# Kernel optimization log

Measured on AMD Instinct MI355X. Metric: run time of the kernel, lower is better.

Reference implementation:

```python
import jax, jax.numpy as jnp
import numpy as np

EMBED = 1024
HEADS = 16
HEAD_DIM = EMBED // HEADS
RANK = 8
ALPHA = 16
SCALE_LORA = ALPHA / RANK  # 2.0


def _lora_linear(x, W, b, A, B):
    # F.linear(x, W, b) + scale * F.linear(F.linear(x, A), B)
    return x @ W.T + b + SCALE_LORA * ((x @ A.T) @ B.T)


def setup_inputs() -> dict:
    key = jax.random.key(0)
    ks = jax.random.split(key, 17)
    d = {"x": jax.random.normal(ks[0], (2, 2048, EMBED), dtype=jnp.float32)}
    names = ["q", "k", "v", "o"]
    i = 1
    for n in names:
        d[f"W{n}"] = jax.random.normal(ks[i], (EMBED, EMBED), dtype=jnp.float32) * 0.02; i += 1
        d[f"b{n}"] = jnp.zeros((EMBED,), dtype=jnp.float32)
        d[f"A{n}"] = jax.random.normal(ks[i], (RANK, EMBED), dtype=jnp.float32) * 0.02; i += 1
        d[f"B{n}"] = jax.random.normal(ks[i], (EMBED, RANK), dtype=jnp.float32) * 0.02; i += 1
    return d


def reference(x, Wq, bq, Aq, Bq, Wk, bk, Ak, Bk, Wv, bv, Av, Bv, Wo, bo, Ao, Bo):
    N, S, _ = x.shape
    Q = _lora_linear(x, Wq, bq, Aq, Bq).reshape(N, S, HEADS, HEAD_DIM)
    K = _lora_linear(x, Wk, bk, Ak, Bk).reshape(N, S, HEADS, HEAD_DIM)
    V = _lora_linear(x, Wv, bv, Av, Bv).reshape(N, S, HEADS, HEAD_DIM)
    # energy: [N, H, Sq, Sk]
    energy = jnp.einsum("nqhd,nkhd->nhqk", Q, K) / jnp.sqrt(jnp.float32(HEAD_DIM))
    attn = jax.nn.softmax(energy, axis=-1)
    out = jnp.einsum("nhqk,nkhd->nqhd", attn, V).reshape(N, S, EMBED)
    return _lora_linear(out, Wo, bo, Ao, Bo)
```

## Files before the change

kernel.cpp:

```cpp
#include <hip/hip_runtime.h>
#include <stdint.h>

typedef uint16_t u16;
typedef short s16x8 __attribute__((ext_vector_type(8)));
typedef float f32x4 __attribute__((ext_vector_type(4)));
typedef unsigned short u16x4 __attribute__((ext_vector_type(4)));
typedef uint32_t u32;
typedef u32 u32x2 __attribute__((ext_vector_type(2)));
typedef u32 u32x4 __attribute__((ext_vector_type(4)));

#define MFMA16(a,b,c) __builtin_amdgcn_mfma_f32_16x16x32_bf16((a),(b),(c),0,0,0)
#define QSCALE 0.18033688011112042f

__device__ __forceinline__ float b2f(u16 b){
  union { u32 u; float f; } v; v.u = ((u32)b)<<16; return v.f;
}
__device__ __forceinline__ u16 f2b(float f){
  union { float f; u32 u; } v; v.f = f;
  return (u16)((v.u + 0x7fffu + ((v.u>>16)&1u))>>16);
}
__device__ __forceinline__ u32 fbits(float f){
  union { float f; u32 u; } v; v.f = f; return v.u;
}
__device__ __forceinline__ void load_lds_16B(const void* g, void* l){
  __builtin_amdgcn_global_load_lds((const __attribute__((address_space(1))) void*)g,
                                   (__attribute__((address_space(3))) void*)l, 16, 0, 0);
}

template<bool XF32, int NMAT>
__global__ __launch_bounds__(256) void lora_conv_kernel(
    const void* __restrict__ Xv,
    const float* __restrict__ A0, const float* __restrict__ A1, const float* __restrict__ A2,
    float* __restrict__ T0, float* __restrict__ T1, float* __restrict__ T2,
    u16* __restrict__ xb,
    const float* __restrict__ W0, const float* __restrict__ W1,
    const float* __restrict__ W2, const float* __restrict__ W3,
    u16* __restrict__ Wb)
{
  if (XF32 && blockIdx.x >= 1024){
    const int cv = blockIdx.x - 1024;
    const int y = cv>>8;
    const float* src = (y==0)?W0:(y==1)?W1:(y==2)?W2:W3;
    u16* dst = Wb + (size_t)y*1048576;
    const int g = (cv&255)*256 + threadIdx.x;
#pragma unroll
    for (int t=0;t<4;t++){
      const int i4 = g + t*65536;
      const f32x4 v = *(const f32x4*)(src + (size_t)i4*4);
      u16x4 o;
#pragma unroll
      for (int j=0;j<4;j++) o[j] = f2b(v[j]);
      *(u16x4*)(dst + (size_t)i4*4) = o;
    }
    return;
  }

  const int wid = threadIdx.x>>6, lane = threadIdx.x&63;
  const int m = blockIdx.x*4 + wid;

  float xf[16];
  if (XF32){
    const float* xp = (const float*)Xv + (size_t)m*1024 + lane*16;
#pragma unroll
    for (int q=0;q<4;q++){
      const f32x4 v = *(const f32x4*)(xp + q*4);
#pragma unroll
      for (int j=0;j<4;j++) xf[q*4+j] = v[j];
    }
    u16* xbp = xb + (size_t)m*1024 + lane*16;
#pragma unroll
    for (int q=0;q<4;q++){
      u16x4 o;
#pragma unroll
      for (int j=0;j<4;j++) o[j] = f2b(xf[q*4+j]);
      *(u16x4*)(xbp + q*4) = o;
    }
  } else {
    const u16* xp = (const u16*)Xv + (size_t)m*1024 + lane*16;
#pragma unroll
    for (int j=0;j<16;j++) xf[j] = b2f(xp[j]);
  }

#pragma unroll
  for (int mat=0; mat<NMAT; mat++){
    const float* A = (mat==0)?A0:(mat==1)?A1:A2;
    float* T = (mat==0)?T0:(mat==1)?T1:T2;
    float accv[8];
#pragma unroll
    for (int r=0;r<8;r++){
      const float* ap = A + r*1024 + lane*16;
      float s = 0.f;
#pragma unroll
      for (int q=0;q<4;q++){
        const f32x4 av = *(const f32x4*)(ap + q*4);
#pragma unroll
        for (int j=0;j<4;j++) s += xf[q*4+j]*av[j];
      }
      accv[r] = s;
    }
#pragma unroll
    for (int r=0;r<8;r++){
      float s = accv[r];
      s += __shfl_xor(s,1);  s += __shfl_xor(s,2);  s += __shfl_xor(s,4);
      s += __shfl_xor(s,8);  s += __shfl_xor(s,16); s += __shfl_xor(s,32);
      accv[r] = s;
    }
    if (lane==0){
#pragma unroll
      for (int r=0;r<8;r++) T[(size_t)m*8 + r] = accv[r];
    }
  }
}

__global__ __launch_bounds__(256,2) void gemm_qkv_kernel(
    const u16* __restrict__ Xb, const u16* __restrict__ Wb,
    const float* __restrict__ bq, const float* __restrict__ bk, const float* __restrict__ bv,
    const float* __restrict__ tq, const float* __restrict__ tk, const float* __restrict__ tv,
    const float* __restrict__ Blq, const float* __restrict__ Blk, const float* __restrict__ Blv,
    u16* __restrict__ Qb, u16* __restrict__ Kb, u16* __restrict__ Vtb)
{
  __shared__ u16 At[128*32];
  __shared__ u16 Bt[128*32];
  const int tid = threadIdx.x;
  const int wid = tid>>6, lane = tid&63;
  const int quad = lane>>4, l16 = lane&15;
  const int wm = wid>>1, wn = wid&1;
  const int proj = blockIdx.x>>3;
  const int n0 = (blockIdx.x&7)<<7, m0 = blockIdx.y<<7;
  const u16* W = Wb + (size_t)proj*1048576;
  const float* bias = (proj==0)?bq:(proj==1)?bk:bv;
  const float* T    = (proj==0)?tq:(proj==1)?tk:tv;
  const float* Bl   = (proj==0)?Blq:(proj==1)?Blk:Blv;
  const float scale = (proj==0)?QSCALE:1.0f;

  f32x4 acc[4][4];
#pragma unroll
  for (int i=0;i<4;i++)
#pragma unroll
    for (int j=0;j<4;j++) acc[i][j] = f32x4{0.f,0.f,0.f,0.f};

  for (int k0=0;k0<1024;k0+=32){
#pragma unroll
    for (int p=0;p<2;p++){
      const int s = wid*128 + p*64 + lane;
      const int row = s>>2, c = s&3;
      load_lds_16B(Xb + (size_t)(m0+row)*1024 + k0 + c*8, At + (wid*128+p*64)*8);
      load_lds_16B(W  + (size_t)(n0+row)*1024 + k0 + c*8, Bt + (wid*128+p*64)*8);
    }
    __syncthreads();
    s16x8 af[4], bfr[4];
#pragma unroll
    for (int t=0;t<4;t++){
      const int r = wm*64 + t*16 + l16;
      af[t]  = *(const s16x8*)(At + r*32 + quad*8);
      const int c = wn*64 + t*16 + l16;
      bfr[t] = *(const s16x8*)(Bt + c*32 + quad*8);
    }
#pragma unroll
    for (int tm=0;tm<4;tm++)
#pragma unroll
      for (int tn=0;tn<4;tn++)
        acc[tm][tn] = MFMA16(af[tm], bfr[tn], acc[tm][tn]);
    __syncthreads();
  }

  s16x8 tf[4], bfl[4];
#pragma unroll
  for (int t=0;t<4;t++){ tf[t] = s16x8{0,0,0,0,0,0,0,0}; bfl[t] = s16x8{0,0,0,0,0,0,0,0}; }
  if (quad==0){
#pragma unroll
    for (int tm=0;tm<4;tm++){
      const float* tp = T + (size_t)(m0 + wm*64 + tm*16 + l16)*8;
      const f32x4 a0 = *(const f32x4*)(tp);
      const f32x4 a1 = *(const f32x4*)(tp+4);
#pragma unroll
      for (int j=0;j<4;j++){ tf[tm][j] = (short)f2b(2.0f*a0[j]); tf[tm][4+j] = (short)f2b(2.0f*a1[j]); }
    }
#pragma unroll
    for (int tn=0;tn<4;tn++){
      const float* bp = Bl + (size_t)(n0 + wn*64 + tn*16 + l16)*8;
      const f32x4 b0 = *(const f32x4*)(bp);
      const f32x4 b1 = *(const f32x4*)(bp+4);
#pragma unroll
      for (int j=0;j<4;j++){ bfl[tn][j] = (short)f2b(b0[j]); bfl[tn][4+j] = (short)f2b(b1[j]); }
    }
  }
#pragma unroll
  for (int tm=0;tm<4;tm++)
#pragma unroll
    for (int tn=0;tn<4;tn++)
      acc[tm][tn] = MFMA16(tf[tm], bfl[tn], acc[tm][tn]);

#pragma unroll
  for (int tn=0;tn<4;tn++){
    const int n = n0 + wn*64 + tn*16 + l16;
    const float bn = bias[n];
#pragma unroll
    for (int tm=0;tm<4;tm++){
      const int mb = m0 + wm*64 + tm*16 + quad*4;
      if (proj==0){
#pragma unroll
        for (int rg=0;rg<4;rg++) Qb[(size_t)(mb+rg)*1024 + n] = f2b((acc[tm][tn][rg]+bn)*scale);
      } else if (proj==1){
#pragma unroll
        for (int rg=0;rg<4;rg++) Kb[(size_t)(mb+rg)*1024 + n] = f2b(acc[tm][tn][rg]+bn);
      } else {
        const int batch = mb>>11, sI = mb&2047;
        const int hh = n>>6, dd = n&63;
        u16x4 pk;
#pragma unroll
        for (int rg=0;rg<4;rg++) pk[rg] = f2b(acc[tm][tn][rg]+bn);
        *(u16x4*)(Vtb + (size_t)((batch*16+hh)*64+dd)*2048 + sI) = pk;
      }
    }
  }
}

__global__ __launch_bounds__(256,2) void gemm_o_kernel(
    const u16* __restrict__ Xb, const u16* __restrict__ W,
    const float* __restrict__ bias, const float* __restrict__ T,
    const float* __restrict__ Bl, float* __restrict__ Out)
{
  __shared__ u16 At[128*32];
  __shared__ u16 Bt[64*32];
  const int tid = threadIdx.x;
  const int wid = tid>>6, lane = tid&63;
  const int quad = lane>>4, l16 = lane&15;
  const int wm = wid>>1, wn = wid&1;
  const int m0 = blockIdx.y<<7, n0 = blockIdx.x<<6;

  f32x4 acc[4][2];
#pragma unroll
  for (int i=0;i<4;i++)
#pragma unroll
    for (int j=0;j<2;j++) acc[i][j] = f32x4{0.f,0.f,0.f,0.f};

  for (int k0=0;k0<1024;k0+=32){
#pragma unroll
    for (int p=0;p<2;p++){
      const int s = wid*128 + p*64 + lane;
      const int row = s>>2, c = s&3;
      load_lds_16B(Xb + (size_t)(m0+row)*1024 + k0 + c*8, At + (wid*128+p*64)*8);
    }
    { const int s = wid*64 + lane;
      const int row = s>>2, c = s&3;
      load_lds_16B(W + (size_t)(n0+row)*1024 + k0 + c*8, Bt + (wid*64)*8); }
    __syncthreads();
    s16x8 af[4], bfr[2];
#pragma unroll
    for (int t=0;t<4;t++){
      const int r = wm*64 + t*16 + l16;
      af[t] = *(const s16x8*)(At + r*32 + quad*8);
    }
#pragma unroll
    for (int t=0;t<2;t++){
      const int c = wn*32 + t*16 + l16;
      bfr[t] = *(const s16x8*)(Bt + c*32 + quad*8);
    }
#pragma unroll
    for (int tm=0;tm<4;tm++)
#pragma unroll
      for (int tn=0;tn<2;tn++)
        acc[tm][tn] = MFMA16(af[tm], bfr[tn], acc[tm][tn]);
    __syncthreads();
  }

  s16x8 tf[4], bfl[2];
#pragma unroll
  for (int t=0;t<4;t++) tf[t] = s16x8{0,0,0,0,0,0,0,0};
#pragma unroll
  for (int t=0;t<2;t++) bfl[t] = s16x8{0,0,0,0,0,0,0,0};
  if (quad==0){
#pragma unroll
    for (int tm=0;tm<4;tm++){
      const float* tp = T + (size_t)(m0 + wm*64 + tm*16 + l16)*8;
      const f32x4 a0 = *(const f32x4*)(tp);
      const f32x4 a1 = *(const f32x4*)(tp+4);
#pragma unroll
      for (int j=0;j<4;j++){ tf[tm][j] = (short)f2b(2.0f*a0[j]); tf[tm][4+j] = (short)f2b(2.0f*a1[j]); }
    }
#pragma unroll
    for (int tn=0;tn<2;tn++){
      const float* bp = Bl + (size_t)(n0 + wn*32 + tn*16 + l16)*8;
      const f32x4 b0 = *(const f32x4*)(bp);
      const f32x4 b1 = *(const f32x4*)(bp+4);
#pragma unroll
      for (int j=0;j<4;j++){ bfl[tn][j] = (short)f2b(b0[j]); bfl[tn][4+j] = (short)f2b(b1[j]); }
    }
  }
#pragma unroll
  for (int tm=0;tm<4;tm++)
#pragma unroll
    for (int tn=0;tn<2;tn++)
      acc[tm][tn] = MFMA16(tf[tm], bfl[tn], acc[tm][tn]);

#pragma unroll
  for (int tn=0;tn<2;tn++){
    const int n = n0 + wn*32 + tn*16 + l16;
    const float bn = bias[n];
#pragma unroll
    for (int tm=0;tm<4;tm++){
      const int mb = m0 + wm*64 + tm*16 + quad*4;
#pragma unroll
      for (int rg=0;rg<4;rg++)
        Out[(size_t)(mb+rg)*1024 + n] = acc[tm][tn][rg] + bn;
    }
  }
}

__global__ __launch_bounds__(512,4) void attn_kernel(
    const u16* __restrict__ Q, const u16* __restrict__ K,
    const u16* __restrict__ Vt, u16* __restrict__ Out)
{
  __shared__ u16 KtB[2][128*72];
  __shared__ u16 VtB[2][64*136];
  const int tid = threadIdx.x;
  const int wid = tid>>6, lane = tid&63;
  const int quad = lane>>4, l16 = lane&15;
  const int q0 = blockIdx.x<<7;
  const int h = blockIdx.y, nb = blockIdx.z;
  const int qg = wid>>1;
  const int kh = wid&1;
  const int qw = qg*32;

  s16x8 qf[2][2];
#pragma unroll
  for (int g=0;g<2;g++){
    const int row = q0 + qw + g*16 + l16;
#pragma unroll
    for (int dh=0;dh<2;dh++)
      qf[g][dh] = *(const s16x8*)(Q + (size_t)(nb*2048+row)*1024 + h*64 + dh*32 + quad*8);
  }
  f32x4 OT[2][4];
  f32x4 Lacc[2];
#pragma unroll
  for (int g=0;g<2;g++){
#pragma unroll
    for (int td=0;td<4;td++) OT[g][td] = f32x4{0.f,0.f,0.f,0.f};
    Lacc[g] = f32x4{0.f,0.f,0.f,0.f};
  }
  s16x8 ones;
#pragma unroll
  for (int j=0;j<8;j++) ones[j] = (short)0x3F80;

  s16x8 kreg[2], vreg[2];
  auto LOADT = [&](int kn){
#pragma unroll
    for (int p=0;p<2;p++){
      const int s = p*512 + tid;
      kreg[p] = *(const s16x8*)(K + (size_t)(nb*2048+kn+(s>>3))*1024 + h*64 + (s&7)*8);
      vreg[p] = *(const s16x8*)(Vt + (size_t)((nb*16+h)*64+(s>>4))*2048 + kn + (s&15)*8);
    }
  };
  auto WRITET = [&](int b){
    u16* Ktb = KtB[b]; u16* Vtb = VtB[b];
#pragma unroll
    for (int p=0;p<2;p++){
      const int s = p*512 + tid;
      *(s16x8*)(Ktb + (s>>3)*72 + (s&7)*8) = kreg[p];
      *(s16x8*)(Vtb + (s>>4)*136 + (s&15)*8) = vreg[p];
    }
  };

  LOADT(0);
  WRITET(0);
  LOADT(128);
  __syncthreads();

  for (int t=0;t<16;t++){
    const int cur = t&1;
    if (t < 15) WRITET(cur^1);
    if (t < 14) LOADT((t+2)*128);
    const u16* KtC = KtB[cur];
    const u16* VtC = VtB[cur];

#pragma unroll
    for (int kb=0;kb<2;kb++){
      u32 ew[2][2], ow[2][2];
#pragma unroll
      for (int sel=0;sel<2;sel++){
        const int key = kh*64 + kb*32 + sel*16 + l16;
        const s16x8 kf0 = *(const s16x8*)(KtC + key*72 + quad*8);
        const s16x8 kf1 = *(const s16x8*)(KtC + key*72 + 32 + quad*8);
#pragma unroll
        for (int g=0;g<2;g++){
          f32x4 z = f32x4{0.f,0.f,0.f,0.f};
          z = MFMA16(kf0, qf[g][0], z);
          z = MFMA16(kf1, qf[g][1], z);
          const float p0 = __builtin_amdgcn_exp2f(z[0]);
          const float p1 = __builtin_amdgcn_exp2f(z[1]);
          const float p2 = __builtin_amdgcn_exp2f(z[2]);
          const float p3 = __builtin_amdgcn_exp2f(z[3]);
          const u32 w0 = __builtin_amdgcn_perm(fbits(p1), fbits(p0), 0x07060302u);
          const u32 w1 = __builtin_amdgcn_perm(fbits(p3), fbits(p2), 0x07060302u);
          if (sel==0){ ew[g][0]=w0; ew[g][1]=w1; } else { ow[g][0]=w0; ow[g][1]=w1; }
        }
      }
      s16x8 pf[2];
#pragma unroll
      for (int g=0;g<2;g++){
        const u32x2 r32 = __builtin_amdgcn_permlane32_swap(ew[g][0], ow[g][0], false, false);
        const u32x2 r16 = __builtin_amdgcn_permlane16_swap(r32[0], r32[1], false, false);
        const u32x2 s32 = __builtin_amdgcn_permlane32_swap(ew[g][1], ow[g][1], false, false);
        const u32x2 s16v = __builtin_amdgcn_permlane16_swap(s32[0], s32[1], false, false);
        u32x4 pw; pw[0]=r16[0]; pw[1]=s16v[0]; pw[2]=r16[1]; pw[3]=s16v[1];
        pf[g] = __builtin_bit_cast(s16x8, pw);
      }
      __builtin_amdgcn_s_setprio(1);
#pragma unroll
      for (int td=0;td<4;td++){
        const s16x8 vf = *(const s16x8*)(VtC + (td*16+l16)*136 + kh*64 + kb*32 + quad*8);
#pragma unroll
        for (int g=0;g<2;g++)
          OT[g][td] = MFMA16(vf, pf[g], OT[g][td]);
      }
#pragma unroll
      for (int g=0;g<2;g++)
        Lacc[g] = MFMA16(ones, pf[g], Lacc[g]);
      __builtin_amdgcn_s_setprio(0);
    }
    __syncthreads();
  }

  float* ep = (float*)KtB;
  float* lw = (float*)VtB;
  if (kh==1){
#pragma unroll
    for (int g=0;g<2;g++){
      const int q = qw + g*16 + l16;
#pragma unroll
      for (int td=0;td<4;td++)
        *(f32x4*)(ep + q*68 + td*16 + quad*4) = OT[g][td];
      if (quad==0) lw[q] = Lacc[g][0];
    }
  }
  __syncthreads();
  if (kh==0){
#pragma unroll
    for (int g=0;g<2;g++){
      const int q = qw + g*16 + l16;
      const float linv = 1.0f / (Lacc[g][0] + lw[q]);
      const int qout = q0 + q;
#pragma unroll
      for (int td=0;td<4;td++){
        const f32x4 o2 = *(const f32x4*)(ep + q*68 + td*16 + quad*4);
        u16x4 pk;
#pragma unroll
        for (int rg=0;rg<4;rg++) pk[rg] = f2b((OT[g][td][rg]+o2[rg])*linv);
        *(u16x4*)(Out + (size_t)(nb*2048+qout)*1024 + h*64 + td*16 + quad*4) = pk;
      }
    }
  }
}

extern "C" void kernel_launch(void* const* d_in, const int* in_sizes, int n_in,
                              void* d_out, int out_size, void* d_ws, size_t ws_size,
                              hipStream_t stream)
{
  const float* x  = (const float*)d_in[0];
  const float* Wq = (const float*)d_in[1];  const float* bq = (const float*)d_in[2];
  const float* Aq = (const float*)d_in[3];  const float* Bq = (const float*)d_in[4];
  const float* Wk = (const float*)d_in[5];  const float* bk = (const float*)d_in[6];
  const float* Ak = (const float*)d_in[7];  const float* Bk = (const float*)d_in[8];
  const float* Wv = (const float*)d_in[9];  const float* bv = (const float*)d_in[10];
  const float* Av = (const float*)d_in[11]; const float* Bv = (const float*)d_in[12];
  const float* Wo = (const float*)d_in[13]; const float* bo = (const float*)d_in[14];
  const float* Ao = (const float*)d_in[15]; const float* Bo = (const float*)d_in[16];

  char* ws = (char*)d_ws;
  float* tq = (float*)(ws + 0);
  float* tk = (float*)(ws + 131072);
  float* tv = (float*)(ws + 262144);
  float* to = (float*)(ws + 393216);
  u16* xb  = (u16*)(ws + 524288);
  u16* Ab  = xb;
  u16* Wb  = (u16*)(ws + 524288 + 8388608);
  u16* Qb  = (u16*)(ws + 524288 + 2*8388608);
  u16* Kb  = (u16*)(ws + 524288 + 3*8388608);
  u16* Vtb = (u16*)(ws + 524288 + 4*8388608);

  lora_conv_kernel<true,3><<<dim3(2048),256,0,stream>>>(
      x, Aq, Ak, Av, tq, tk, tv, xb, Wq, Wk, Wv, Wo, Wb);
  gemm_qkv_kernel<<<dim3(24,32),256,0,stream>>>(xb, Wb, bq, bk, bv, tq, tk, tv,
                                                Bq, Bk, Bv, Qb, Kb, Vtb);
  attn_kernel<<<dim3(16,16,2),512,0,stream>>>(Qb, Kb, Vtb, Ab);
  lora_conv_kernel<false,1><<<dim3(1024),256,0,stream>>>(
      Ab, Ao, Ao, Ao, to, to, to, nullptr,
      nullptr, nullptr, nullptr, nullptr, nullptr);
  gemm_o_kernel<<<dim3(16,32),256,0,stream>>>(Ab, Wb + (size_t)3*1048576, bo, to, Bo,
                                              (float*)d_out);
}
```

Baseline: 238.6 us.

## Deepen GEMM K-step to 64, stage V transpose via LDS, swizzle attention blocks

Both projection GEMMs now load two 32-wide K slices per iteration, which halves the number of barrier pairs over the K loop at the cost of more LDS. The V projection epilogue first writes its tile into LDS transposed and then stores 16-byte coalesced rows to the transposed V buffer, replacing scattered 8-byte writes. The attention kernel remaps its block index with a swizzle so that consecutively launched blocks are spread across heads and batches, which changes how they land on XCDs and caches.

New measurement: 229.1 us. 4.0% less time.

```diff
diff --git a/kernel.cpp b/kernel.cpp
--- a/kernel.cpp
+++ b/kernel.cpp
@@ -119,8 +119,9 @@
     const float* __restrict__ Blq, const float* __restrict__ Blk, const float* __restrict__ Blv,
     u16* __restrict__ Qb, u16* __restrict__ Kb, u16* __restrict__ Vtb)
 {
-  __shared__ u16 At[128*32];
-  __shared__ u16 Bt[128*32];
+  __shared__ u16 sm[16896];
+  u16* AtB = sm;
+  u16* BtB = sm + 8192;
   const int tid = threadIdx.x;
   const int wid = tid>>6, lane = tid&63;
   const int quad = lane>>4, l16 = lane&15;
@@ -139,28 +140,34 @@
 #pragma unroll
     for (int j=0;j<4;j++) acc[i][j] = f32x4{0.f,0.f,0.f,0.f};
 
-  for (int k0=0;k0<1024;k0+=32){
-#pragma unroll
-    for (int p=0;p<2;p++){
-      const int s = wid*128 + p*64 + lane;
-      const int row = s>>2, c = s&3;
-      load_lds_16B(Xb + (size_t)(m0+row)*1024 + k0 + c*8, At + (wid*128+p*64)*8);
-      load_lds_16B(W  + (size_t)(n0+row)*1024 + k0 + c*8, Bt + (wid*128+p*64)*8);
+  for (int k0=0;k0<1024;k0+=64){
+#pragma unroll
+    for (int half=0; half<2; half++){
+#pragma unroll
+      for (int p=0;p<2;p++){
+        const int s = wid*128 + p*64 + lane;
+        const int row = s>>2, c = s&3;
+        load_lds_16B(Xb + (size_t)(m0+row)*1024 + k0 + half*32 + c*8, AtB + half*4096 + (wid*128+p*64)*8);
+        load_lds_16B(W  + (size_t)(n0+row)*1024 + k0 + half*32 + c*8, BtB + half*4096 + (wid*128+p*64)*8);
+      }
     }
     __syncthreads();
-    s16x8 af[4], bfr[4];
-#pragma unroll
-    for (int t=0;t<4;t++){
-      const int r = wm*64 + t*16 + l16;
-      af[t]  = *(const s16x8*)(At + r*32 + quad*8);
-      const int c = wn*64 + t*16 + l16;
-      bfr[t] = *(const s16x8*)(Bt + c*32 + quad*8);
-    }
-#pragma unroll
-    for (int tm=0;tm<4;tm++)
-#pragma unroll
-      for (int tn=0;tn<4;tn++)
-        acc[tm][tn] = MFMA16(af[tm], bfr[tn], acc[tm][tn]);
+#pragma unroll
+    for (int half=0; half<2; half++){
+      s16x8 af[4], bfr[4];
+#pragma unroll
+      for (int t=0;t<4;t++){
+        const int r = wm*64 + t*16 + l16;
+        af[t]  = *(const s16x8*)(AtB + half*4096 + r*32 + quad*8);
+        const int c = wn*64 + t*16 + l16;
+        bfr[t] = *(const s16x8*)(BtB + half*4096 + c*32 + quad*8);
+      }
+#pragma unroll
+      for (int tm=0;tm<4;tm++)
+#pragma unroll
+        for (int tn=0;tn<4;tn++)
+          acc[tm][tn] = MFMA16(af[tm], bfr[tn], acc[tm][tn]);
+    }
     __syncthreads();
   }
 
@@ -191,26 +198,45 @@
     for (int tn=0;tn<4;tn++)
       acc[tm][tn] = MFMA16(tf[tm], bfl[tn], acc[tm][tn]);
 
-#pragma unroll
-  for (int tn=0;tn<4;tn++){
-    const int n = n0 + wn*64 + tn*16 + l16;
-    const float bn = bias[n];
-#pragma unroll
-    for (int tm=0;tm<4;tm++){
-      const int mb = m0 + wm*64 + tm*16 + quad*4;
-      if (proj==0){
-#pragma unroll
-        for (int rg=0;rg<4;rg++) Qb[(size_t)(mb+rg)*1024 + n] = f2b((acc[tm][tn][rg]+bn)*scale);
-      } else if (proj==1){
-#pragma unroll
-        for (int rg=0;rg<4;rg++) Kb[(size_t)(mb+rg)*1024 + n] = f2b(acc[tm][tn][rg]+bn);
-      } else {
-        const int batch = mb>>11, sI = mb&2047;
-        const int hh = n>>6, dd = n&63;
+  if (proj==2){
+#pragma unroll
+    for (int tn=0;tn<4;tn++){
+      const int nl = wn*64 + tn*16 + l16;
+      const float bn = bias[n0+nl];
+#pragma unroll
+      for (int tm=0;tm<4;tm++){
+        const int ml = wm*64 + tm*16 + quad*4;
         u16x4 pk;
 #pragma unroll
         for (int rg=0;rg<4;rg++) pk[rg] = f2b(acc[tm][tn][rg]+bn);
-        *(u16x4*)(Vtb + (size_t)((batch*16+hh)*64+dd)*2048 + sI) = pk;
+        *(u16x4*)(sm + nl*132 + ml) = pk;
+      }
+    }
+    __syncthreads();
+    const int batch = m0>>11, sbase = m0&2047;
+#pragma unroll
+    for (int p=0;p<8;p++){
+      const int idx = p*256 + tid;
+      const int row = idx>>4, c16 = idx&15;
+      const s16x8 v = *(const s16x8*)(sm + row*132 + c16*8);
+      const int ng = n0 + row, hh = ng>>6, dd = ng&63;
+      *(s16x8*)(Vtb + (size_t)((batch*16+hh)*64+dd)*2048 + sbase + c16*8) = v;
+    }
+  } else {
+#pragma unroll
+    for (int tn=0;tn<4;tn++){
+      const int n = n0 + wn*64 + tn*16 + l16;
+      const float bn = bias[n];
+#pragma unroll
+      for (int tm=0;tm<4;tm++){
+        const int mb = m0 + wm*64 + tm*16 + quad*4;
+        if (proj==0){
+#pragma unroll
+          for (int rg=0;rg<4;rg++) Qb[(size_t)(mb+rg)*1024 + n] = f2b((acc[tm][tn][rg]+bn)*scale);
+        } else {
+#pragma unroll
+          for (int rg=0;rg<4;rg++) Kb[(size_t)(mb+rg)*1024 + n] = f2b(acc[tm][tn][rg]+bn);
+        }
       }
     }
   }
@@ -221,8 +247,8 @@
     const float* __restrict__ bias, const float* __restrict__ T,
     const float* __restrict__ Bl, float* __restrict__ Out)
 {
-  __shared__ u16 At[128*32];
-  __shared__ u16 Bt[64*32];
+  __shared__ u16 At[2][128*32];
+  __shared__ u16 Bt[2][64*32];
   const int tid = threadIdx.x;
   const int wid = tid>>6, lane = tid&63;
   const int quad = lane>>4, l16 = lane&15;
@@ -235,33 +261,39 @@
 #pragma unroll
     for (int j=0;j<2;j++) acc[i][j] = f32x4{0.f,0.f,0.f,0.f};
 
-  for (int k0=0;k0<1024;k0+=32){
-#pragma unroll
-    for (int p=0;p<2;p++){
-      const int s = wid*128 + p*64 + lane;
-      const int row = s>>2, c = s&3;
-      load_lds_16B(Xb + (size_t)(m0+row)*1024 + k0 + c*8, At + (wid*128+p*64)*8);
-    }
-    { const int s = wid*64 + lane;
-      const int row = s>>2, c = s&3;
-      load_lds_16B(W + (size_t)(n0+row)*1024 + k0 + c*8, Bt + (wid*64)*8); }
+  for (int k0=0;k0<1024;k0+=64){
+#pragma unroll
+    for (int half=0; half<2; half++){
+#pragma unroll
+      for (int p=0;p<2;p++){
+        const int s = wid*128 + p*64 + lane;
+        const int row = s>>2, c = s&3;
+        load_lds_16B(Xb + (size_t)(m0+row)*1024 + k0 + half*32 + c*8, At[half] + (wid*128+p*64)*8);
+      }
+      { const int s = wid*64 + lane;
+        const int row = s>>2, c = s&3;
+        load_lds_16B(W + (size_t)(n0+row)*1024 + k0 + half*32 + c*8, Bt[half] + (wid*64)*8); }
+    }
     __syncthreads();
-    s16x8 af[4], bfr[2];
-#pragma unroll
-    for (int t=0;t<4;t++){
-      const int r = wm*64 + t*16 + l16;
-      af[t] = *(const s16x8*)(At + r*32 + quad*8);
-    }
-#pragma unroll
-    for (int t=0;t<2;t++){
-      const int c = wn*32 + t*16 + l16;
-      bfr[t] = *(const s16x8*)(Bt + c*32 + quad*8);
-    }
-#pragma unroll
-    for (int tm=0;tm<4;tm++)
-#pragma unroll
-      for (int tn=0;tn<2;tn++)
-        acc[tm][tn] = MFMA16(af[tm], bfr[tn], acc[tm][tn]);
+#pragma unroll
+    for (int half=0; half<2; half++){
+      s16x8 af[4], bfr[2];
+#pragma unroll
+      for (int t=0;t<4;t++){
+        const int r = wm*64 + t*16 + l16;
+        af[t] = *(const s16x8*)(At[half] + r*32 + quad*8);
+      }
+#pragma unroll
+      for (int t=0;t<2;t++){
+        const int c = wn*32 + t*16 + l16;
+        bfr[t] = *(const s16x8*)(Bt[half] + c*32 + quad*8);
+      }
+#pragma unroll
+      for (int tm=0;tm<4;tm++)
+#pragma unroll
+        for (int tn=0;tn<2;tn++)
+          acc[tm][tn] = MFMA16(af[tm], bfr[tn], acc[tm][tn]);
+    }
     __syncthreads();
   }
 
@@ -317,8 +349,11 @@
   const int tid = threadIdx.x;
   const int wid = tid>>6, lane = tid&63;
   const int quad = lane>>4, l16 = lane&15;
-  const int q0 = blockIdx.x<<7;
-  const int h = blockIdx.y, nb = blockIdx.z;
+  const int lin = blockIdx.x + (blockIdx.y<<4) + (blockIdx.z<<8);
+  const int swz = (lin&7)*64 + (lin>>3);
+  const int q0 = (swz&15)<<7;
+  const int h  = (swz>>4)&15;
+  const int nb = swz>>8;
   const int qg = wid>>1;
   const int kh = wid&1;
   const int qw = qg*32;
```
